# Performance work log

Hardware: AMD Instinct MI355X
Metric: run time of the kernel (lower is better)

## Reference

```python
import jax, jax.numpy as jnp
import numpy as np
from jax.scipy import special

B, N, DIM, H, DK, DV, F = 2, 1536, 1536, 8, 64, 64, 192


def _pos_embed(seq_len, feat):
    """Enformer relative positional basis: [2*seq_len-1, feat]."""
    per = feat // 6  # 3 basis families x (symmetric, antisymmetric)
    d = jnp.arange(-seq_len + 1, seq_len, dtype=jnp.float32)
    ad = jnp.abs(d)[:, None]  # [2N-1, 1]
    # exponential decay, log-spaced half lives
    half_life = 2.0 ** jnp.linspace(3.0, float(np.log2(seq_len)), per)
    expo = jnp.exp(-jnp.log(2.0) / half_life * ad)
    # central binary mask
    widths = 2.0 ** jnp.arange(1, per + 1, dtype=jnp.float32) - 1.0
    cmask = (widths > ad).astype(jnp.float32)
    # gamma pdf basis
    stddev = seq_len / (2.0 * per)
    start_mean = seq_len / per
    mean = jnp.linspace(start_mean, float(seq_len), per)
    conc = (mean / stddev) ** 2
    rate = mean / stddev ** 2
    log_unnorm = special.xlogy(conc - 1.0, ad) - rate * ad
    log_norm = special.gammaln(conc) - conc * jnp.log(rate)
    probs = jnp.exp(log_unnorm - log_norm) + 1e-8
    gamma = probs / jnp.max(probs, axis=-1, keepdims=True)
    emb = jnp.concatenate([expo, cmask, gamma], axis=-1)
    emb = jnp.concatenate([emb, jnp.sign(d)[:, None] * emb], axis=-1)
    return emb.astype(jnp.float32)


def _relative_shift(x):
    # x: [B, H, N, 2N-1] -> [B, H, N, N] (Transformer-XL shift)
    b, h, t1, t2 = x.shape
    x = jnp.pad(x, ((0, 0), (0, 0), (0, 0), (1, 0)))  # [B,H,N,2N]
    x = x.reshape(b, h, t2 + 1, t1)[:, :, 1:, :].reshape(b, h, t1, t2)
    return x[..., : (t2 + 2) // 2]


def setup_inputs() -> dict:
    key = jax.random.key(0)
    ks = jax.random.split(key, 8)
    s = 0.02
    return {
        "x": jax.random.normal(ks[0], (B, N, DIM), dtype=jnp.float32),
        "Wq": jax.random.normal(ks[1], (DIM, H * DK), dtype=jnp.float32) * s,
        "Wk": jax.random.normal(ks[2], (DIM, H * DK), dtype=jnp.float32) * s,
        "Wv": jax.random.normal(ks[3], (DIM, H * DV), dtype=jnp.float32) * s,
        "Wrel": jax.random.normal(ks[4], (F, H * DK), dtype=jnp.float32) * s,
        "Wout": jax.random.normal(ks[5], (H * DV, DIM), dtype=jnp.float32) * s,
        "bout": jnp.zeros((DIM,), dtype=jnp.float32),
        "rel_content_bias": jax.random.normal(ks[6], (1, H, 1, DK), dtype=jnp.float32),
        "rel_pos_bias": jax.random.normal(ks[7], (1, H, 1, DK), dtype=jnp.float32),
        "pos_embed": _pos_embed(N, F),  # [2N-1, F] buffer
    }


def reference(x, Wq, Wk, Wv, Wrel, Wout, bout, rel_content_bias, rel_pos_bias, pos_embed):
    b, n, _ = x.shape
    h, dk = rel_content_bias.shape[1], rel_content_bias.shape[3]
    dv = Wv.shape[1] // h
    scale = dk ** -0.5
    q = (x @ Wq).reshape(b, n, h, dk).transpose(0, 2, 1, 3) * scale  # [b,h,n,dk]
    k = (x @ Wk).reshape(b, n, h, dk).transpose(0, 2, 1, 3)
    v = (x @ Wv).reshape(b, n, h, dv).transpose(0, 2, 1, 3)
    content_logits = jnp.einsum('bhid,bhjd->bhij', q + rel_content_bias, k)
    rel_k = (pos_embed @ Wrel).reshape(-1, h, dk).transpose(1, 0, 2)  # [h,2n-1,dk]
    rel_logits = jnp.einsum('bhid,hjd->bhij', q + rel_pos_bias, rel_k)  # [b,h,n,2n-1]
    rel_logits = _relative_shift(rel_logits)  # [b,h,n,n]
    attn = jax.nn.softmax(content_logits + rel_logits, axis=-1)
    out = jnp.einsum('bhij,bhjd->bhid', attn, v)
    out = out.transpose(0, 2, 1, 3).reshape(b, n, h * dv)
    return out @ Wout + bout
```

## Files before the change

### kernel.cpp

```cpp
#include <hip/hip_runtime.h>

#define NSEQ  1536
#define HEADS 8
#define NREL  3071
#define NRELP 3072

typedef __bf16 bf16;
typedef __bf16 bf16x8 __attribute__((ext_vector_type(8)));
typedef __bf16 bf16x4 __attribute__((ext_vector_type(4)));
typedef float  f32x4  __attribute__((ext_vector_type(4)));

static __device__ __forceinline__ f32x4 mfma16(bf16x8 a, bf16x8 b, f32x4 c) {
  return __builtin_amdgcn_mfma_f32_16x16x32_bf16(a, b, c, 0, 0, 0);
}

static __device__ __forceinline__ void gload_lds16(const bf16* g, bf16* l) {
  __builtin_amdgcn_global_load_lds((const __attribute__((address_space(1))) void*)g,
                                   (__attribute__((address_space(3))) void*)l, 16, 0, 0);
}

#define DPP_F(v, ctrl) __int_as_float(__builtin_amdgcn_update_dpp(0, __float_as_int(v), ctrl, 0xF, 0xF, true))
static __device__ __forceinline__ float rowsum16(float v) {
  v += DPP_F(v, 0xB1);
  v += DPP_F(v, 0x4E);
  v += DPP_F(v, 0x124);
  v += DPP_F(v, 0x128);
  return v;
}

__global__ __launch_bounds__(256) void prep(const float* __restrict__ x, const float* __restrict__ pos,
                                            const float* __restrict__ Wq, const float* __restrict__ Wk,
                                            const float* __restrict__ Wv, const float* __restrict__ Wout,
                                            const float* __restrict__ Wrel,
                                            bf16* __restrict__ xb, bf16* __restrict__ posb,
                                            bf16* __restrict__ WT, bf16* __restrict__ WoT,
                                            bf16* __restrict__ WrT) {
  int blk = blockIdx.x;
  if (blk < 4608) {
    int i = blk * 256 + threadIdx.x;
    float4 v = ((const float4*)x)[i];
    bf16x4 o;
    o[0] = (bf16)v.x; o[1] = (bf16)v.y; o[2] = (bf16)v.z; o[3] = (bf16)v.w;
    ((bf16x4*)xb)[i] = o;
    return;
  }
  blk -= 4608;
  if (blk < 576) {
    int i = blk * 256 + threadIdx.x;
    if (i < (NREL * 192 / 4)) {
      float4 v = ((const float4*)pos)[i];
      bf16x4 o;
      o[0] = (bf16)v.x; o[1] = (bf16)v.y; o[2] = (bf16)v.z; o[3] = (bf16)v.w;
      ((bf16x4*)posb)[i] = o;
    }
    return;
  }
  blk -= 576;
  const float* in; bf16* out; int C, ostride, orowoff, cx, ry;
  if (blk < 768)       { in = Wq;   out = WT;  C = 512;  ostride = 1536; orowoff = 0;    cx = blk % 16; ry = blk / 16; }
  else if (blk < 1536) { blk -= 768;  in = Wk;   out = WT;  C = 512;  ostride = 1536; orowoff = 512;  cx = blk % 16; ry = blk / 16; }
  else if (blk < 2304) { blk -= 1536; in = Wv;   out = WT;  C = 512;  ostride = 1536; orowoff = 1024; cx = blk % 16; ry = blk / 16; }
  else if (blk < 3072) { blk -= 2304; in = Wout; out = WoT; C = 1536; ostride = 512;  orowoff = 0;    cx = blk % 48; ry = blk / 48; }
  else                 { blk -= 3072; in = Wrel; out = WrT; C = 512;  ostride = 192;  orowoff = 0;    cx = blk % 16; ry = blk / 16; }
  __shared__ float t[32][33];
  int tx = threadIdx.x & 31, ty = threadIdx.x >> 5;
  int r0 = ry * 32, c0 = cx * 32;
#pragma unroll
  for (int i = 0; i < 4; i++)
    t[ty + 8 * i][tx] = in[(size_t)(r0 + ty + 8 * i) * C + c0 + tx];
  __syncthreads();
#pragma unroll
  for (int i = 0; i < 4; i++)
    out[(size_t)(c0 + ty + 8 * i + orowoff) * ostride + r0 + tx] = (bf16)t[tx][ty + 8 * i];
}

static __device__ __forceinline__ void gemm_core(const bf16* __restrict__ A, const bf16* __restrict__ BT,
                                                 int Klen, int ldk, int m0, int n0, int M,
                                                 bf16* sa, bf16* sb, f32x4 acc[4][2]) {
  int tid = threadIdx.x, wave = tid >> 6, lane = tid & 63;
  int l15 = lane & 15, quad = lane >> 4;
  int lrow = lane >> 3, lcg = lane & 7;
  for (int k0 = 0; k0 < Klen; k0 += 64) {
    __syncthreads();
#pragma unroll
    for (int t = 0; t < 2; t++) {
      int row = wave * 16 + t * 8 + lrow;
      int ra = m0 + row; if (ra > M - 1) ra = M - 1;
      gload_lds16(A + (size_t)ra * ldk + k0 + ((lcg ^ (row & 7)) * 8), sa + (wave * 16 + t * 8) * 64);
    }
#pragma unroll
    for (int t = 0; t < 4; t++) {
      int row = wave * 32 + t * 8 + lrow;
      gload_lds16(BT + (size_t)(n0 + row) * ldk + k0 + ((lcg ^ (row & 7)) * 8), sb + (wave * 32 + t * 8) * 64);
    }
    __syncthreads();
#pragma unroll
    for (int kq = 0; kq < 2; kq++) {
      bf16x8 af[4], bfr[2];
#pragma unroll
      for (int rt = 0; rt < 4; rt++) {
        int row = rt * 16 + l15;
        af[rt] = *(const bf16x8*)&sa[row * 64 + (((kq * 4 + quad) ^ (row & 7)) * 8)];
      }
#pragma unroll
      for (int ct = 0; ct < 2; ct++) {
        int row = wave * 32 + ct * 16 + l15;
        bfr[ct] = *(const bf16x8*)&sb[row * 64 + (((kq * 4 + quad) ^ (row & 7)) * 8)];
      }
#pragma unroll
      for (int ct = 0; ct < 2; ct++)
#pragma unroll
        for (int rt = 0; rt < 4; rt++)
          acc[rt][ct] = mfma16(af[rt], bfr[ct], acc[rt][ct]);
    }
  }
}

__global__ __launch_bounds__(256) void gemm_qkvrel(const bf16* __restrict__ xb, const bf16* __restrict__ WT,
                                                   const bf16* __restrict__ posb, const bf16* __restrict__ WrT,
                                                   const float* __restrict__ cb, const float* __restrict__ pb,
                                                   bf16* __restrict__ qc, bf16* __restrict__ qp,
                                                   bf16* __restrict__ kb, bf16* __restrict__ vt,
                                                   bf16* __restrict__ rk) {
  __shared__ __align__(16) bf16 sa[64 * 64];
  __shared__ __align__(16) bf16 sb[128 * 64];
  __shared__ __align__(16) bf16 tv[64 * 130];
  int tid = threadIdx.x, wave = tid >> 6, lane = tid & 63;
  int l15 = lane & 15, quad = lane >> 4;
  int m0 = blockIdx.x * 64;
  f32x4 acc[4][2] = {};
  if (blockIdx.y >= 12) {
    int n0 = (blockIdx.y - 12) * 128;
    gemm_core(posb, WrT, 192, 192, m0, n0, NREL, sa, sb, acc);
#pragma unroll
    for (int rt = 0; rt < 4; rt++)
#pragma unroll
      for (int ct = 0; ct < 2; ct++)
#pragma unroll
        for (int r = 0; r < 4; r++) {
          int row = m0 + rt * 16 + quad * 4 + r;
          if (row < NREL) {
            int col = n0 + wave * 32 + ct * 16 + l15;
            rk[((size_t)(col >> 6) * NRELP + row) * 64 + (col & 63)] = (bf16)acc[rt][ct][r];
          }
        }
    return;
  }
  int n0 = blockIdx.y * 128;
  gemm_core(xb, WT, 1536, 1536, m0, n0, 3072, sa, sb, acc);
  int b = m0 / NSEQ, nseq0 = m0 % NSEQ;
  if (blockIdx.y < 8) {
    bool isq = blockIdx.y < 4;
#pragma unroll
    for (int rt = 0; rt < 4; rt++)
#pragma unroll
      for (int ct = 0; ct < 2; ct++)
#pragma unroll
        for (int r = 0; r < 4; r++) {
          int row = nseq0 + rt * 16 + quad * 4 + r;
          int colg = n0 + wave * 32 + ct * 16 + l15;
          int col = colg & 511;
          int h = col >> 6, d = col & 63;
          size_t o = ((size_t)(b * 8 + h) * NSEQ + row) * 64 + d;
          float v = acc[rt][ct][r];
          if (isq) {
            float qv = v * 0.18033688011f;
            qc[o] = (bf16)(qv + cb[col] * 1.44269504089f);
            qp[o] = (bf16)(qv + pb[col] * 1.44269504089f);
          } else {
            kb[o] = (bf16)v;
          }
        }
  } else {
#pragma unroll
    for (int rt = 0; rt < 4; rt++)
#pragma unroll
      for (int ct = 0; ct < 2; ct++)
#pragma unroll
        for (int r = 0; r < 4; r++)
          tv[(rt * 16 + quad * 4 + r) * 130 + wave * 32 + ct * 16 + l15] = (bf16)acc[rt][ct][r];
    __syncthreads();
    int n = tid & 63, c0v = tid >> 6;
    int hbase = (blockIdx.y - 8) * 2;
#pragma unroll
    for (int hh = 0; hh < 2; hh++)
#pragma unroll
      for (int i = 0; i < 16; i++) {
        int dv = i * 4 + c0v;
        vt[((size_t)(b * 8 + hbase + hh) * 64 + dv) * NSEQ + nseq0 + n] = tv[n * 130 + hh * 64 + dv];
      }
  }
}

__global__ __launch_bounds__(256) void gemm_out(const bf16* __restrict__ A, const bf16* __restrict__ BT,
                                                float* __restrict__ C, const float* __restrict__ bias) {
  __shared__ __align__(16) bf16 sa[64 * 64];
  __shared__ __align__(16) bf16 sb[128 * 64];
  int tid = threadIdx.x, wave = tid >> 6, lane = tid & 63;
  int l15 = lane & 15, quad = lane >> 4;
  int m0 = blockIdx.x * 64, n0 = blockIdx.y * 128;
  f32x4 acc[4][2] = {};
  gemm_core(A, BT, 512, 512, m0, n0, 3072, sa, sb, acc);
#pragma unroll
  for (int rt = 0; rt < 4; rt++)
#pragma unroll
    for (int ct = 0; ct < 2; ct++)
#pragma unroll
      for (int r = 0; r < 4; r++) {
        int row = m0 + rt * 16 + quad * 4 + r;
        int col = n0 + wave * 32 + ct * 16 + l15;
        C[(size_t)row * 1536 + col] = acc[rt][ct][r] + bias[col];
      }
}

__global__ __launch_bounds__(256, 4) void attn(const bf16* __restrict__ qc, const bf16* __restrict__ qp,
                                               const bf16* __restrict__ kb, const bf16* __restrict__ vt,
                                               const bf16* __restrict__ rk,
                                               float* __restrict__ Opart, float* __restrict__ mlp) {
  __shared__ __align__(16) bf16 sk[64 * 64];
  __shared__ __align__(16) bf16 sv[64 * 64];
  __shared__ __align__(16) bf16 srel[128 * 64];
  __shared__ __align__(16) bf16 pls[4][16 * 64];
  int qb = blockIdx.x, bh = blockIdx.y, kz = blockIdx.z;
  int h = bh & 7;
  int i0 = qb * 64;
  int wave = threadIdx.x >> 6, lane = threadIdx.x & 63;
  int l15 = lane & 15, quad = lane >> 4;
  int lrow = lane >> 3, lcg = lane & 7;
  const bf16* qcb = qc + (size_t)bh * NSEQ * 64;
  const bf16* qpb = qp + (size_t)bh * NSEQ * 64;
  const bf16* kbb = kb + (size_t)bh * NSEQ * 64;
  const bf16* vtb = vt + (size_t)bh * 64 * NSEQ;
  const bf16* rkh = rk + (size_t)h * NRELP * 64;
  bf16* plsw = pls[wave];

  int qrow = i0 + wave * 16 + l15;
  bf16x8 aqc0 = *(const bf16x8*)(qcb + (size_t)qrow * 64 + quad * 8);
  bf16x8 aqc1 = *(const bf16x8*)(qcb + (size_t)qrow * 64 + 32 + quad * 8);
  bf16x8 aqp0 = *(const bf16x8*)(qpb + (size_t)qrow * 64 + quad * 8);
  bf16x8 aqp1 = *(const bf16x8*)(qpb + (size_t)qrow * 64 + 32 + quad * 8);

  int bidx[4];
  bool hisel[4];
#pragma unroll
  for (int r = 0; r < 4; r++) {
    int rl = quad * 4 + r;
    bidx[r] = (quad * 16 + ((l15 + 15 - rl) & 15)) << 2;
    hisel[r] = l15 > rl;
  }

  int swz = (lcg ^ lrow) * 8;
  int jb = 23 + kz * 12 - qb;
  const bf16* pK = kbb + (size_t)(kz * 768 + wave * 16 + lrow) * 64 + swz;
  const bf16* pV = vtb + (size_t)(wave * 16 + lrow) * NSEQ + kz * 768 + swz;
  const bf16* pR = rkh + (size_t)(jb + 1) * 4096 + (size_t)(wave * 16 + lrow) * 64 + swz;
  bf16* wK = sk + (wave * 16 + lrow) * 64 + lcg * 8;
  bf16* wV = sv + (wave * 16 + lrow) * 64 + lcg * 8;
  int wRoff = (wave * 16 + lrow) * 64 + lcg * 8;

  {
    const bf16* pP = rkh + (size_t)jb * 4096 + (size_t)(wave * 16 + lrow) * 64 + swz;
    bf16* dP = srel + ((jb & 1) * 64 + wave * 16) * 64;
#pragma unroll
    for (int t = 0; t < 2; t++)
      gload_lds16(pP + t * 512, dP + t * 512);
  }
  float4 kr0 = *(const float4*)(pK), kr1 = *(const float4*)(pK + 512);             pK += 4096;
  float4 vr0 = *(const float4*)(pV), vr1 = *(const float4*)(pV + 8 * NSEQ);        pV += 64;
  float4 rr0 = *(const float4*)(pR), rr1 = *(const float4*)(pR + 512);             pR += 4096;
  int pxor = (jb & 1) << 6;

  int swzA = (quad ^ (l15 & 7)) * 8;
  int swzB = ((4 + quad) ^ (l15 & 7)) * 8;
  int rb0 = (3 - wave) * 16 + l15;
  int pxl = (l15 >> 1) << 3;
  const bf16* plr = plsw + l15 * 64;

  f32x4 acco[4] = {};
  float li[4] = {0.0f, 0.0f, 0.0f, 0.0f};

  for (int jt = 0; jt < 12; jt++) {
    __syncthreads();
    *(float4*)(wK) = kr0;        *(float4*)(wK + 512) = kr1;
    *(float4*)(wV) = vr0;        *(float4*)(wV + 512) = vr1;
    {
      bf16* wR = srel + (pxor ^ 64) * 64 + wRoff;
      *(float4*)(wR) = rr0;      *(float4*)(wR + 512) = rr1;
    }
    __syncthreads();
    if (jt < 11) {
      kr0 = *(const float4*)(pK); kr1 = *(const float4*)(pK + 512);        pK += 4096;
      vr0 = *(const float4*)(pV); vr1 = *(const float4*)(pV + 8 * NSEQ);   pV += 64;
      rr0 = *(const float4*)(pR); rr1 = *(const float4*)(pR + 512);        pR += 4096;
    }
    f32x4 s[4] = {};
#pragma unroll
    for (int c = 0; c < 4; c++) {
      const bf16* kp = sk + (c * 16 + l15) * 64;
      s[c] = mfma16(aqc0, *(const bf16x8*)(kp + swzA), s[c]);
      s[c] = mfma16(aqc1, *(const bf16x8*)(kp + swzB), s[c]);
    }
    f32x4 sb5[5];
#pragma unroll
    for (int cc = 0; cc < 5; cc++) {
      const bf16* rp = srel + ((rb0 + cc * 16) ^ pxor) * 64;
      f32x4 z = {};
      z = mfma16(aqp0, *(const bf16x8*)(rp + swzA), z);
      sb5[cc] = mfma16(aqp1, *(const bf16x8*)(rp + swzB), z);
    }
#pragma unroll
    for (int r = 0; r < 4; r++) {
      float bp[5];
#pragma unroll
      for (int cc = 0; cc < 5; cc++)
        bp[cc] = __int_as_float(__builtin_amdgcn_ds_bpermute(bidx[r], __float_as_int(sb5[cc][r])));
#pragma unroll
      for (int c = 0; c < 4; c++)
        s[c][r] += hisel[r] ? bp[c + 1] : bp[c];
    }
#pragma unroll
    for (int c = 0; c < 4; c++)
#pragma unroll
      for (int r = 0; r < 4; r++) {
        float p = __builtin_amdgcn_exp2f(s[c][r] - 11.5415603f);
        bf16 pbh = (bf16)p;
        li[r] += (float)pbh;
        int prow = quad * 4 + r;
        plsw[prow * 64 + ((c * 16 + l15) ^ ((prow >> 1) << 3))] = pbh;
      }
#pragma unroll
    for (int ks = 0; ks < 2; ks++) {
      bf16x8 ap = *(const bf16x8*)(plr + ((ks * 32 + quad * 8) ^ pxl));
#pragma unroll
      for (int c = 0; c < 4; c++) {
        const bf16* vp = sv + (c * 16 + l15) * 64;
        acco[c] = mfma16(ap, *(const bf16x8*)(vp + (ks ? swzB : swzA)), acco[c]);
      }
    }
    pxor ^= 64;
  }
#pragma unroll
  for (int r = 0; r < 4; r++)
    li[r] = rowsum16(li[r]);
  int qt16 = qb * 4 + wave;
  size_t pbase = ((size_t)(bh * 96 + qt16) * 2 + kz);
#pragma unroll
  for (int c = 0; c < 4; c++)
#pragma unroll
    for (int r = 0; r < 4; r++)
      Opart[pbase * 1024 + (quad * 4 + r) * 64 + c * 16 + l15] = acco[c][r];
  if (l15 == 0) {
#pragma unroll
    for (int r = 0; r < 4; r++)
      mlp[pbase * 16 + quad * 4 + r] = li[r];
  }
}

__global__ void attn_merge(const float* __restrict__ Opart, const float* __restrict__ mlp,
                           bf16* __restrict__ O) {
  int qt = blockIdx.x, bh = blockIdx.y;
  int b = bh >> 3, h = bh & 7;
  int col = threadIdx.x & 63, rg = threadIdx.x >> 6;
  size_t base = (size_t)(bh * 96 + qt) * 2;
#pragma unroll
  for (int rr = 0; rr < 4; rr++) {
    int row = rg * 4 + rr;
    float L = mlp[base * 16 + row] + mlp[(base + 1) * 16 + row];
    float v = Opart[base * 1024 + row * 64 + col] + Opart[(base + 1) * 1024 + row * 64 + col];
    O[((size_t)(b * NSEQ + qt * 16 + row) * 8 + h) * 64 + col] = (bf16)(v / L);
  }
}

extern "C" void kernel_launch(void* const* d_in, const int* in_sizes, int n_in,
                              void* d_out, int out_size, void* d_ws, size_t ws_size,
                              hipStream_t stream) {
  const float* x    = (const float*)d_in[0];
  const float* Wq   = (const float*)d_in[1];
  const float* Wk   = (const float*)d_in[2];
  const float* Wv   = (const float*)d_in[3];
  const float* Wrel = (const float*)d_in[4];
  const float* Wout = (const float*)d_in[5];
  const float* bout = (const float*)d_in[6];
  const float* cb   = (const float*)d_in[7];
  const float* pb   = (const float*)d_in[8];
  const float* pos  = (const float*)d_in[9];
  float* out = (float*)d_out;

  char* ws = (char*)d_ws;
  size_t off = 0;
  auto alloc = [&](size_t bytes) {
    char* p = ws + off;
    off = (off + bytes + 255) & ~(size_t)255;
    return p;
  };
  bf16*  xb    = (bf16*)alloc(3072UL * 1536 * 2);
  bf16*  WT    = (bf16*)alloc(1536UL * 1536 * 2);
  bf16*  WoT   = (bf16*)alloc(1536UL * 512 * 2);
  bf16*  WrT   = (bf16*)alloc(512UL * 192 * 2);
  bf16*  posb  = (bf16*)alloc((size_t)NREL * 192 * 2);
  bf16*  qcb   = (bf16*)alloc(16UL * NSEQ * 64 * 2);
  bf16*  qpb   = (bf16*)alloc(16UL * NSEQ * 64 * 2);
  bf16*  kbb   = (bf16*)alloc(16UL * NSEQ * 64 * 2);
  bf16*  vtb   = (bf16*)alloc(16UL * NSEQ * 64 * 2);
  bf16*  rkb   = (bf16*)alloc(8UL * NRELP * 64 * 2);
  bf16*  Ob    = (bf16*)alloc(3072UL * 512 * 2);
  float* Opart = (float*)alloc(16UL * 96 * 2 * 1024 * 4);
  float* mlpw  = (float*)alloc(16UL * 96 * 2 * 16 * 4);

  prep<<<dim3(8352), 256, 0, stream>>>(x, pos, Wq, Wk, Wv, Wout, Wrel, xb, posb, WT, WoT, WrT);
  gemm_qkvrel<<<dim3(48, 16), 256, 0, stream>>>(xb, WT, posb, WrT, cb, pb, qcb, qpb, kbb, vtb, rkb);
  attn<<<dim3(24, 16, 2), 256, 0, stream>>>(qcb, qpb, kbb, vtb, rkb, Opart, mlpw);
  attn_merge<<<dim3(96, 16), 256, 0, stream>>>(Opart, mlpw, Ob);
  gemm_out<<<dim3(48, 12), 256, 0, stream>>>(Ob, WoT, out, bout);
}
```

Before: 171.2 us.

## Register-prefetch next GEMM k-tile instead of direct global-to-LDS loads

Replaces the synchronous global_load_lds tile fills in the shared GEMM core with register prefetching. The next k-tile is loaded into registers while MFMAs run on the current LDS tile, then written to LDS after the barrier. Swizzle offsets are precomputed outside the loop. This hides global load latency behind compute, at the cost of extra VGPRs and explicit LDS store instructions.

After: 174.4 us. No clear change (+1.9%).

```diff
diff --git a/kernel.cpp b/kernel.cpp
--- a/kernel.cpp
+++ b/kernel.cpp
@@ -80,33 +80,54 @@
   int tid = threadIdx.x, wave = tid >> 6, lane = tid & 63;
   int l15 = lane & 15, quad = lane >> 4;
   int lrow = lane >> 3, lcg = lane & 7;
+  int swz = (lcg ^ lrow) * 8;
+
+  int rowA = wave * 16 + lrow;
+  int ra0 = m0 + rowA;     if (ra0 > M - 1) ra0 = M - 1;
+  int ra1 = m0 + rowA + 8; if (ra1 > M - 1) ra1 = M - 1;
+  const bf16* pA0 = A + (size_t)ra0 * ldk + swz;
+  const bf16* pA1 = A + (size_t)ra1 * ldk + swz;
+  int rowB = wave * 32 + lrow;
+  const bf16* pB = BT + (size_t)(n0 + rowB) * ldk + swz;
+  size_t ldk8 = (size_t)ldk * 8;
+  bf16* wA = sa + rowA * 64 + lcg * 8;
+  bf16* wB = sb + rowB * 64 + lcg * 8;
+
+  float4 a0 = *(const float4*)pA0;
+  float4 a1 = *(const float4*)pA1;
+  float4 b0 = *(const float4*)(pB);
+  float4 b1 = *(const float4*)(pB + ldk8);
+  float4 b2 = *(const float4*)(pB + 2 * ldk8);
+  float4 b3 = *(const float4*)(pB + 3 * ldk8);
+
+  int swzA = (quad ^ (l15 & 7)) * 8;
+  int swzB = ((4 + quad) ^ (l15 & 7)) * 8;
+
   for (int k0 = 0; k0 < Klen; k0 += 64) {
     __syncthreads();
-#pragma unroll
-    for (int t = 0; t < 2; t++) {
-      int row = wave * 16 + t * 8 + lrow;
-      int ra = m0 + row; if (ra > M - 1) ra = M - 1;
-      gload_lds16(A + (size_t)ra * ldk + k0 + ((lcg ^ (row & 7)) * 8), sa + (wave * 16 + t * 8) * 64);
-    }
-#pragma unroll
-    for (int t = 0; t < 4; t++) {
-      int row = wave * 32 + t * 8 + lrow;
-      gload_lds16(BT + (size_t)(n0 + row) * ldk + k0 + ((lcg ^ (row & 7)) * 8), sb + (wave * 32 + t * 8) * 64);
-    }
+    *(float4*)(wA) = a0;        *(float4*)(wA + 512) = a1;
+    *(float4*)(wB) = b0;        *(float4*)(wB + 512) = b1;
+    *(float4*)(wB + 1024) = b2; *(float4*)(wB + 1536) = b3;
     __syncthreads();
+    if (k0 + 64 < Klen) {
+      pA0 += 64; pA1 += 64; pB += 64;
+      a0 = *(const float4*)pA0;
+      a1 = *(const float4*)pA1;
+      b0 = *(const float4*)(pB);
+      b1 = *(const float4*)(pB + ldk8);
+      b2 = *(const float4*)(pB + 2 * ldk8);
+      b3 = *(const float4*)(pB + 3 * ldk8);
+    }
 #pragma unroll
     for (int kq = 0; kq < 2; kq++) {
       bf16x8 af[4], bfr[2];
-#pragma unroll
-      for (int rt = 0; rt < 4; rt++) {
-        int row = rt * 16 + l15;
-        af[rt] = *(const bf16x8*)&sa[row * 64 + (((kq * 4 + quad) ^ (row & 7)) * 8)];
-      }
-#pragma unroll
-      for (int ct = 0; ct < 2; ct++) {
-        int row = wave * 32 + ct * 16 + l15;
-        bfr[ct] = *(const bf16x8*)&sb[row * 64 + (((kq * 4 + quad) ^ (row & 7)) * 8)];
-      }
+      int sz = kq ? swzB : swzA;
+#pragma unroll
+      for (int rt = 0; rt < 4; rt++)
+        af[rt] = *(const bf16x8*)&sa[(rt * 16 + l15) * 64 + sz];
+#pragma unroll
+      for (int ct = 0; ct < 2; ct++)
+        bfr[ct] = *(const bf16x8*)&sb[(wave * 32 + ct * 16 + l15) * 64 + sz];
 #pragma unroll
       for (int ct = 0; ct < 2; ct++)
 #pragma unroll
```
